# Kernel tuning notes

Hardware: AMD Instinct MI355X
Metric: run time of the kernel (lower is better)

## Reference

```python
import jax, jax.numpy as jnp
import numpy as np
from jax import lax

D_MODEL, D_STATE, D_CONV, EXPAND = 1024, 16, 4, 2
D_INNER = EXPAND * D_MODEL
B, L = 2, 2048


def setup_inputs() -> dict:
    key = jax.random.key(0)
    ks = jax.random.split(key, 8)
    s_in = 1.0 / np.sqrt(D_MODEL)
    s_xp = 1.0 / np.sqrt(D_INNER)
    x = jax.random.normal(ks[0], (B, L, D_MODEL), dtype=jnp.float32)
    W_in = jax.random.uniform(ks[1], (2 * D_INNER, D_MODEL), minval=-s_in, maxval=s_in)
    conv_w = jax.random.uniform(ks[2], (D_INNER, 1, D_CONV), minval=-0.5, maxval=0.5)
    conv_b = jax.random.uniform(ks[3], (D_INNER,), minval=-0.5, maxval=0.5)
    W_xproj = jax.random.uniform(ks[4], (1 + 2 * D_STATE, D_INNER), minval=-s_xp, maxval=s_xp)
    W_dt = jax.random.uniform(ks[5], (D_INNER, 1), minval=-1.0, maxval=1.0)
    b_dt = jax.random.uniform(ks[6], (D_INNER,), minval=-1.0, maxval=1.0)
    A_log = jnp.log(jnp.broadcast_to(jnp.arange(1, D_STATE + 1, dtype=jnp.float32), (D_INNER, D_STATE)))
    D = jnp.ones((D_INNER,), dtype=jnp.float32)
    W_out = jax.random.uniform(ks[7], (D_MODEL, D_INNER), minval=-s_xp, maxval=s_xp)
    return {"x": x, "W_in": W_in, "conv_w": conv_w, "conv_b": conv_b,
            "W_xproj": W_xproj, "W_dt": W_dt, "b_dt": b_dt,
            "A_log": A_log, "D": D, "W_out": W_out}


def reference(x, W_in, conv_w, conv_b, W_xproj, W_dt, b_dt, A_log, D, W_out):
    b, l, _ = x.shape
    d_state = A_log.shape[1]
    d_conv = conv_w.shape[-1]

    xz = x @ W_in.T                                  # (B, L, 2*d_inner)
    x_in, z = jnp.split(xz, 2, axis=-1)

    # causal depthwise conv: torch pads both sides then truncates to [:L]
    lhs = jnp.pad(x_in.transpose(0, 2, 1), ((0, 0), (0, 0), (d_conv - 1, 0)))  # (B, d_inner, L+pad)
    conv = lax.conv_general_dilated(
        lhs, conv_w, window_strides=(1,), padding='VALID',
        dimension_numbers=('NCW', 'OIW', 'NCW'),
        feature_group_count=conv_w.shape[0])
    x_conv = jax.nn.silu(conv.transpose(0, 2, 1) + conv_b)  # (B, L, d_inner)

    ssm_in = x_conv @ W_xproj.T                      # (B, L, 1+2*d_state)
    dt_raw = ssm_in[..., :1]
    B_ssm = ssm_in[..., 1:1 + d_state]               # (B, L, d_state)
    C_ssm = ssm_in[..., 1 + d_state:]                # (B, L, d_state)

    delta = jax.nn.softplus(dt_raw @ W_dt.T + b_dt)  # (B, L, d_inner)
    A = -jnp.exp(A_log)                              # (d_inner, d_state)
    deltaA = jnp.exp(delta[..., None] * A)           # (B, L, d_inner, d_state)
    deltaB_u = delta[..., None] * B_ssm[:, :, None, :] * x_conv[..., None]

    def step(h, inp):
        dA, dBu, c = inp                              # (B,d_inner,d_state)x2, (B,d_state)
        h = dA * h + dBu
        y = jnp.einsum('bds,bs->bd', h, c)
        return h, y

    h0 = jnp.zeros((b, deltaA.shape[2], d_state), dtype=x.dtype)
    _, ys = lax.scan(step, h0, (deltaA.transpose(1, 0, 2, 3),
                                deltaB_u.transpose(1, 0, 2, 3),
                                C_ssm.transpose(1, 0, 2)))
    y = ys.transpose(1, 0, 2) + x_conv * D           # (B, L, d_inner)
    y = y * jax.nn.silu(z)
    return y @ W_out.T
```

## Files before the change

kernel.cpp:

```cpp
#include <hip/hip_runtime.h>
#include <hip/hip_bf16.h>
#include <math.h>

#define D_MODEL 1024
#define D_STATE 16
#define D_CONV  4
#define D_INNER 2048
#define BB      2
#define LL      2048
#define BLROWS  (BB*LL)
#define NCHUNK  64
#define CHUNK   (LL/NCHUNK)
#define SSML    36
#define XSPLIT  16

typedef __hip_bfloat16 bf16;
typedef __attribute__((ext_vector_type(8))) short short8;
typedef __attribute__((ext_vector_type(4))) float f32x4;

__device__ __forceinline__ float ldf(const void* p, long i, int isbf) {
    return isbf ? __bfloat162float(((const bf16*)p)[i]) : ((const float*)p)[i];
}
__device__ __forceinline__ short bfbits(float f) {
    bf16 h = __float2bfloat16(f);
    return *(short*)&h;
}
__device__ __forceinline__ float bits2f(short s) {
    bf16 h; *(short*)&h = s; return __bfloat162float(h);
}
__device__ __forceinline__ float bf2f(bf16 h) { return __bfloat162float(h); }
__device__ __forceinline__ float siluf(float x) {
    return __fdividef(x, 1.f + __expf(-x));
}
__device__ __forceinline__ void softplus_r(float x, float& delta, float& r) {
    float e = __expf(-fabsf(x));
    float t = 1.f + e;
    delta = fmaxf(x, 0.f) + __logf(t);
    r = __fdividef((x >= 0.f) ? e : 1.f, t);
}

#define OFF_CW   0
#define OFF_CB   8192
#define OFF_WDT  10240
#define OFF_BDT  12288
#define OFF_AA   14336
#define OFF_D    47104
#define N_SMALL  49152
#define N_WXPB   (128*2048)
#define N_SSMZ   (BLROWS*SSML)

#define G_LDS16(gptr, lptr) __builtin_amdgcn_global_load_lds( \
    (const __attribute__((address_space(1))) void*)(gptr),    \
    (__attribute__((address_space(3))) void*)(lptr), 16, 0, 0)

__global__ void dtype_probe(const unsigned short* __restrict__ alog, int* __restrict__ flag) {
    if (threadIdx.x == 0) { flag[0] = (alog[1] != 0) ? 1 : 0; flag[1] = 1; }
}

__global__ __launch_bounds__(256) void cvt_prep(
    const void* __restrict__ Wxp, const void* __restrict__ cw,
    const void* __restrict__ cb, const void* __restrict__ wdt,
    const void* __restrict__ bdt, const void* __restrict__ alog,
    const void* __restrict__ Dp,
    bf16* __restrict__ wxpb, float* __restrict__ smallf,
    float* __restrict__ ssm, int* __restrict__ flag)
{
    const int isbf = flag[0];
    int idx = blockIdx.x * 256 + threadIdx.x;
    if (idx < N_WXPB) {
        int row = idx >> 11, col = idx & 2047;
        float v = (row < 33) ? ldf(Wxp, (long)row*2048 + col, isbf) : 0.f;
        wxpb[idx] = __float2bfloat16(v);
        return;
    }
    int j = idx - N_WXPB;
    if      (j < 8192)  smallf[OFF_CW  + j]         = ldf(cw,  j, isbf);
    else if (j < 10240) smallf[OFF_CB  + j - 8192]  = ldf(cb,  j - 8192, isbf);
    else if (j < 12288) smallf[OFF_WDT + j - 10240] = ldf(wdt, j - 10240, isbf);
    else if (j < 14336) smallf[OFF_BDT + j - 12288] = ldf(bdt, j - 12288, isbf);
    else if (j < 47104) {
        int jj = j - 14336;
        float aa = -__expf(ldf(alog, jj, isbf));
        smallf[OFF_AA + jj] = aa;
        int s = jj & 15;
        if (fabsf(aa + (float)(s+1)) > 1e-3f) flag[1] = 0;
    }
    else if (j < 49152) smallf[OFF_D   + j - 47104] = ldf(Dp,  j - 47104, isbf);
    else {
        int z = j - N_SMALL;
        if (z < N_SSMZ) ssm[z] = 0.f;
    }
}

__global__ __launch_bounds__(256) void cvt_all(
    const void* __restrict__ x, const void* __restrict__ win,
    const void* __restrict__ wout,
    bf16* __restrict__ xb, bf16* __restrict__ winb, bf16* __restrict__ woutb,
    const int* __restrict__ flagp)
{
    const int isbf = *flagp;
    int i = blockIdx.x * 256 + threadIdx.x;
    const void* src; bf16* dst; long o;
    if (i < 524288)       { src = x;    dst = xb;    o = (long)i * 8; }
    else if (i < 1048576) { src = win;  dst = winb;  o = (long)(i - 524288) * 8; }
    else if (i < 1310720) { src = wout; dst = woutb; o = (long)(i - 1048576) * 8; }
    else return;
    short8 v;
    if (isbf) {
        v = *(const short8*)((const bf16*)src + o);
    } else {
        const float* s = (const float*)src + o;
        f32x4 u = *(const f32x4*)s, w = *(const f32x4*)(s + 4);
        v[0]=bfbits(u[0]); v[1]=bfbits(u[1]); v[2]=bfbits(u[2]); v[3]=bfbits(u[3]);
        v[4]=bfbits(w[0]); v[5]=bfbits(w[1]); v[6]=bfbits(w[2]); v[7]=bfbits(w[3]);
    }
    *(short8*)(dst + o) = v;
}

__global__ __launch_bounds__(512) void gemm8p(
    const bf16* __restrict__ A,
    const bf16* __restrict__ Bm,
    bf16* __restrict__ Cp)
{
    __shared__ bf16 As[2][256*64];
    __shared__ bf16 Bs[2][256*64];
    const int t    = threadIdx.x;
    const int lane = t & 63;
    const int wm   = (t >> 6) >> 2;
    const int wn   = (t >> 6) & 3;
    const int bm   = blockIdx.y, bn = blockIdx.x;
    const int quad = lane >> 4, l16 = lane & 15;
    const int NST  = 16;

    f32x4 acc[8][4];
    #pragma unroll
    for (int i = 0; i < 8; i++)
        #pragma unroll
        for (int j = 0; j < 4; j++)
            acc[i][j] = f32x4{0.f, 0.f, 0.f, 0.f};

    auto stage = [&](int bufi, int kt) {
        #pragma unroll
        for (int seg = 0; seg < 4; seg++) {
            int s = seg*512 + t, row = s >> 3, sg = s & 7;
            int col = (sg ^ (row & 7)) * 8;
            G_LDS16(A + ((long)bm*256 + row)*1024 + kt*64 + col, &As[bufi][s*8]);
        }
        #pragma unroll
        for (int seg = 0; seg < 4; seg++) {
            int s = seg*512 + t, row = s >> 3, sg = s & 7;
            int col = (sg ^ (row & 7)) * 8;
            G_LDS16(Bm + ((long)bn*256 + row)*1024 + kt*64 + col, &Bs[bufi][s*8]);
        }
    };

    stage(0, 0);
    stage(1, 1);
    asm volatile("s_waitcnt vmcnt(8)" ::: "memory");
    __builtin_amdgcn_s_barrier();

    int cur = 0;
    for (int t0 = 0; t0 < NST; ++t0) {
        short8 af[2][8], bfv[2][4];
        #pragma unroll
        for (int kk = 0; kk < 2; kk++) {
            #pragma unroll
            for (int rt = 0; rt < 8; rt++) {
                int row = wm*128 + rt*16 + l16;
                int c = kk*4 + quad;
                af[kk][rt] = *(const short8*)&As[cur][row*64 + ((c ^ (row & 7))*8)];
            }
            #pragma unroll
            for (int ct = 0; ct < 4; ct++) {
                int row = wn*64 + ct*16 + l16;
                int c = kk*4 + quad;
                bfv[kk][ct] = *(const short8*)&Bs[cur][row*64 + ((c ^ (row & 7))*8)];
            }
        }
        asm volatile("s_waitcnt lgkmcnt(0)" ::: "memory");
        __builtin_amdgcn_sched_barrier(0);
        __builtin_amdgcn_s_barrier();
        __builtin_amdgcn_sched_barrier(0);
        if (t0 + 2 < NST) stage(cur, t0 + 2);
        __builtin_amdgcn_s_setprio(1);
        #pragma unroll
        for (int kk = 0; kk < 2; kk++)
            #pragma unroll
            for (int rt = 0; rt < 8; rt++)
                #pragma unroll
                for (int ct = 0; ct < 4; ct++)
                    acc[rt][ct] = __builtin_amdgcn_mfma_f32_16x16x32_bf16(
                        af[kk][rt], bfv[kk][ct], acc[rt][ct], 0, 0, 0);
        __builtin_amdgcn_s_setprio(0);
        __builtin_amdgcn_sched_barrier(0);
        if (t0 + 2 < NST) { asm volatile("s_waitcnt vmcnt(8)" ::: "memory"); }
        else              { asm volatile("s_waitcnt vmcnt(0)" ::: "memory"); }
        __builtin_amdgcn_sched_barrier(0);
        __builtin_amdgcn_s_barrier();
        cur ^= 1;
    }

    #pragma unroll
    for (int rt = 0; rt < 8; rt++)
        #pragma unroll
        for (int ct = 0; ct < 4; ct++)
            #pragma unroll
            for (int r = 0; r < 4; r++) {
                int row = bm*256 + wm*128 + rt*16 + quad*4 + r;
                int col = bn*256 + wn*64 + ct*16 + l16;
                Cp[(long)row * 4096 + col] = __float2bfloat16(acc[rt][ct][r]);
            }
}

__global__ __launch_bounds__(256) void gemm_dual(
    const void* __restrict__ A, int lda,
    const void* __restrict__ Bm, int ldb,
    void* __restrict__ Cp, int ldc, int K,
    const int* __restrict__ flagp, int amode, int bmode, int cmode)
{
    const int isbf = *flagp;
    const int a_bf = amode ? isbf : 1;
    const int b_bf = bmode ? isbf : 1;
    const int c_bf = cmode ? isbf : 1;

    __shared__ bf16 As[128*64];
    __shared__ bf16 Bs[128*64];
    const int t    = threadIdx.x;
    const int lane = t & 63;
    const int w    = t >> 6;
    const int wm   = w >> 1, wn = w & 1;
    const int bm   = blockIdx.y, bn = blockIdx.x;
    const int quad = lane >> 4, l16 = lane & 15;

    f32x4 acc[4][4];
    #pragma unroll
    for (int i = 0; i < 4; i++)
        #pragma unroll
        for (int j = 0; j < 4; j++)
            acc[i][j] = f32x4{0.f, 0.f, 0.f, 0.f};

    for (int k0 = 0; k0 < K; k0 += 64) {
        __syncthreads();
        if (a_bf) {
            #pragma unroll
            for (int seg = 0; seg < 4; seg++) {
                int s = seg*256 + t, row = s >> 3, sg = s & 7;
                int col = (sg ^ (row & 7)) * 8;
                const bf16* ga = (const bf16*)A + ((long)bm*128 + row)*(long)lda + k0 + col;
                G_LDS16(ga, &As[row*64 + sg*8]);
            }
        } else {
            #pragma unroll
            for (int seg = 0; seg < 4; seg++) {
                int s = seg*256 + t, row = s >> 3, sg = s & 7;
                int col = (sg ^ (row & 7)) * 8;
                const float* ap = (const float*)A + ((long)bm*128 + row)*(long)lda + k0 + col;
                f32x4 u = *(const f32x4*)ap, v = *(const f32x4*)(ap + 4);
                short8 va;
                va[0]=bfbits(u[0]); va[1]=bfbits(u[1]); va[2]=bfbits(u[2]); va[3]=bfbits(u[3]);
                va[4]=bfbits(v[0]); va[5]=bfbits(v[1]); va[6]=bfbits(v[2]); va[7]=bfbits(v[3]);
                *(short8*)&As[row*64 + sg*8] = va;
            }
        }
        if (b_bf) {
            #pragma unroll
            for (int seg = 0; seg < 4; seg++) {
                int s = seg*256 + t, row = s >> 3, sg = s & 7;
                int col = (sg ^ (row & 7)) * 8;
                const bf16* gb = (const bf16*)Bm + ((long)bn*128 + row)*(long)ldb + k0 + col;
                G_LDS16(gb, &Bs[row*64 + sg*8]);
            }
        } else {
            #pragma unroll
            for (int seg = 0; seg < 4; seg++) {
                int s = seg*256 + t, row = s >> 3, sg = s & 7;
                int col = (sg ^ (row & 7)) * 8;
                const float* bp = (const float*)Bm + ((long)bn*128 + row)*(long)ldb + k0 + col;
                f32x4 u = *(const f32x4*)bp, v = *(const f32x4*)(bp + 4);
                short8 vb;
                vb[0]=bfbits(u[0]); vb[1]=bfbits(u[1]); vb[2]=bfbits(u[2]); vb[3]=bfbits(u[3]);
                vb[4]=bfbits(v[0]); vb[5]=bfbits(v[1]); vb[6]=bfbits(v[2]); vb[7]=bfbits(v[3]);
                *(short8*)&Bs[row*64 + sg*8] = vb;
            }
        }
        __syncthreads();

        #pragma unroll
        for (int kk = 0; kk < 64; kk += 32) {
            const int cbase = kk >> 3;
            short8 af[4], bfr[4];
            #pragma unroll
            for (int mi = 0; mi < 4; mi++) {
                int row = wm*64 + mi*16 + l16;
                int c = cbase + quad;
                af[mi] = *(const short8*)&As[row*64 + ((c ^ (row & 7))*8)];
            }
            #pragma unroll
            for (int ni = 0; ni < 4; ni++) {
                int row = wn*64 + ni*16 + l16;
                int c = cbase + quad;
                bfr[ni] = *(const short8*)&Bs[row*64 + ((c ^ (row & 7))*8)];
            }
            #pragma unroll
            for (int mi = 0; mi < 4; mi++)
                #pragma unroll
                for (int ni = 0; ni < 4; ni++)
                    acc[mi][ni] = __builtin_amdgcn_mfma_f32_16x16x32_bf16(
                        af[mi], bfr[ni], acc[mi][ni], 0, 0, 0);
        }
    }

    #pragma unroll
    for (int mi = 0; mi < 4; mi++)
        #pragma unroll
        for (int ni = 0; ni < 4; ni++)
            #pragma unroll
            for (int r = 0; r < 4; r++) {
                int row = bm*128 + wm*64 + mi*16 + quad*4 + r;
                int col = bn*128 + wn*64 + ni*16 + l16;
                float val = acc[mi][ni][r];
                if (c_bf) ((bf16*)Cp)[(long)row * ldc + col] = __float2bfloat16(val);
                else      ((float*)Cp)[(long)row * ldc + col] = val;
            }
}

__global__ __launch_bounds__(256) void gemm_n64(
    const bf16* __restrict__ A, int lda,
    const void* __restrict__ Bm, int ldb,
    void* __restrict__ Cp, int ldc, int K,
    const int* __restrict__ flagp, int bmode, int cmode)
{
    const int isbf = *flagp;
    const int b_bf = bmode ? isbf : 1;
    const int c_bf = cmode ? isbf : 1;

    __shared__ bf16 As[128*64];
    __shared__ bf16 Bs[64*64];
    const int t    = threadIdx.x;
    const int lane = t & 63;
    const int w    = t >> 6;
    const int wm   = w >> 1, wn = w & 1;
    const int bm   = blockIdx.y, bn = blockIdx.x;
    const int quad = lane >> 4, l16 = lane & 15;

    f32x4 acc[4][2];
    #pragma unroll
    for (int i = 0; i < 4; i++)
        #pragma unroll
        for (int j = 0; j < 2; j++)
            acc[i][j] = f32x4{0.f, 0.f, 0.f, 0.f};

    for (int k0 = 0; k0 < K; k0 += 64) {
        __syncthreads();
        #pragma unroll
        for (int seg = 0; seg < 4; seg++) {
            int s = seg*256 + t, row = s >> 3, sg = s & 7;
            int col = (sg ^ (row & 7)) * 8;
            const bf16* ga = A + ((long)bm*128 + row)*(long)lda + k0 + col;
            G_LDS16(ga, &As[row*64 + sg*8]);
        }
        if (b_bf) {
            #pragma unroll
            for (int seg = 0; seg < 2; seg++) {
                int s = seg*256 + t, row = s >> 3, sg = s & 7;
                int col = (sg ^ (row & 7)) * 8;
                const bf16* gb = (const bf16*)Bm + ((long)bn*64 + row)*(long)ldb + k0 + col;
                G_LDS16(gb, &Bs[row*64 + sg*8]);
            }
        } else {
            #pragma unroll
            for (int seg = 0; seg < 2; seg++) {
                int s = seg*256 + t, row = s >> 3, sg = s & 7;
                int col = (sg ^ (row & 7)) * 8;
                const float* bp = (const float*)Bm + ((long)bn*64 + row)*(long)ldb + k0 + col;
                f32x4 u = *(const f32x4*)bp, v = *(const f32x4*)(bp + 4);
                short8 vb;
                vb[0]=bfbits(u[0]); vb[1]=bfbits(u[1]); vb[2]=bfbits(u[2]); vb[3]=bfbits(u[3]);
                vb[4]=bfbits(v[0]); vb[5]=bfbits(v[1]); vb[6]=bfbits(v[2]); vb[7]=bfbits(v[3]);
                *(short8*)&Bs[row*64 + sg*8] = vb;
            }
        }
        __syncthreads();

        #pragma unroll
        for (int kk = 0; kk < 64; kk += 32) {
            const int cbase = kk >> 3;
            short8 af[4], bfr[2];
            #pragma unroll
            for (int mi = 0; mi < 4; mi++) {
                int row = wm*64 + mi*16 + l16;
                int c = cbase + quad;
                af[mi] = *(const short8*)&As[row*64 + ((c ^ (row & 7))*8)];
            }
            #pragma unroll
            for (int ni = 0; ni < 2; ni++) {
                int row = wn*32 + ni*16 + l16;
                int c = cbase + quad;
                bfr[ni] = *(const short8*)&Bs[row*64 + ((c ^ (row & 7))*8)];
            }
            #pragma unroll
            for (int mi = 0; mi < 4; mi++)
                #pragma unroll
                for (int ni = 0; ni < 2; ni++)
                    acc[mi][ni] = __builtin_amdgcn_mfma_f32_16x16x32_bf16(
                        af[mi], bfr[ni], acc[mi][ni], 0, 0, 0);
        }
    }

    #pragma unroll
    for (int mi = 0; mi < 4; mi++)
        #pragma unroll
        for (int ni = 0; ni < 2; ni++)
            #pragma unroll
            for (int r = 0; r < 4; r++) {
                int row = bm*128 + wm*64 + mi*16 + quad*4 + r;
                int col = bn*64 + wn*32 + ni*16 + l16;
                float val = acc[mi][ni][r];
                if (c_bf) ((bf16*)Cp)[(long)row * ldc + col] = __float2bfloat16(val);
                else      ((float*)Cp)[(long)row * ldc + col] = val;
            }
}

__global__ __launch_bounds__(256) void xproj_fused(
    const bf16* __restrict__ xz, const bf16* __restrict__ wxpb,
    const float* __restrict__ smallf, float* __restrict__ ssm)
{
    const float* cwf = smallf + OFF_CW;
    const float* cbf = smallf + OFF_CB;
    __shared__ bf16 As[128*32];
    __shared__ bf16 Bs[128*32];
    const int t    = threadIdx.x;
    const int lane = t & 63;
    const int w    = t >> 6;
    const int wm   = w >> 1, wn = w & 1;
    const int bm   = blockIdx.y;
    const int ks   = blockIdx.x * (D_INNER / XSPLIT);
    const int quad = lane >> 4, l16 = lane & 15;

    f32x4 acc[4][4];
    #pragma unroll
    for (int i = 0; i < 4; i++)
        #pragma unroll
        for (int j = 0; j < 4; j++)
            acc[i][j] = f32x4{0.f, 0.f, 0.f, 0.f};

    for (int k0 = ks; k0 < ks + D_INNER/XSPLIT; k0 += 32) {
        __syncthreads();
        #pragma unroll
        for (int seg = 0; seg < 2; seg++) {
            int s = seg*256 + t, row = s >> 2, dcol = (s & 3) * 8;
            int blg = bm*128 + row;
            int b = blg >> 11, l = blg & (LL - 1);
            int d0 = k0 + dcol;
            float a[8];
            {
                f32x4 c0 = *(const f32x4*)&cbf[d0], c1 = *(const f32x4*)&cbf[d0+4];
                a[0]=c0[0]; a[1]=c0[1]; a[2]=c0[2]; a[3]=c0[3];
                a[4]=c1[0]; a[5]=c1[1]; a[6]=c1[2]; a[7]=c1[3];
            }
            f32x4 cw4[8];
            #pragma unroll
            for (int j = 0; j < 8; j++) cw4[j] = *(const f32x4*)&cwf[(d0+j)*4];
            #pragma unroll
            for (int kk = 0; kk < D_CONV; kk++) {
                int ls = l - 3 + kk;
                if (ls >= 0) {
                    short8 xv = *(const short8*)&xz[((long)(b*LL + ls))*4096 + d0];
                    #pragma unroll
                    for (int j = 0; j < 8; j++) a[j] += bits2f(xv[j]) * cw4[j][kk];
                }
            }
            short8 va;
            #pragma unroll
            for (int j = 0; j < 8; j++) va[j] = bfbits(siluf(a[j]));
            *(short8*)&As[row*32 + dcol] = va;
        }
        #pragma unroll
        for (int seg = 0; seg < 2; seg++) {
            int s = seg*256 + t, row = s >> 2, col = (s & 3) * 8;
            const bf16* gb = wxpb + (long)row*D_INNER + k0 + col;
            G_LDS16(gb, &Bs[row*32 + col]);
        }
        __syncthreads();

        short8 af[4], bfr[4];
        #pragma unroll
        for (int mi = 0; mi < 4; mi++)
            af[mi] = *(const short8*)&As[(wm*64 + mi*16 + l16)*32 + quad*8];
        #pragma unroll
        for (int ni = 0; ni < 4; ni++)
            bfr[ni] = *(const short8*)&Bs[(wn*64 + ni*16 + l16)*32 + quad*8];
        #pragma unroll
        for (int mi = 0; mi < 4; mi++)
            #pragma unroll
            for (int ni = 0; ni < 4; ni++)
                acc[mi][ni] = __builtin_amdgcn_mfma_f32_16x16x32_bf16(
                    af[mi], bfr[ni], acc[mi][ni], 0, 0, 0);
    }

    #pragma unroll
    for (int mi = 0; mi < 4; mi++)
        #pragma unroll
        for (int ni = 0; ni < 4; ni++) {
            int col = wn*64 + ni*16 + l16;
            if (col < 33) {
                int newcol = (col == 0) ? 32 : (col - 1);
                #pragma unroll
                for (int r = 0; r < 4; r++) {
                    int row = bm*128 + wm*64 + mi*16 + quad*4 + r;
                    atomicAdd(&ssm[(long)row * SSML + newcol], acc[mi][ni][r]);
                }
            }
        }
}

template<int CHUNK_T>
__global__ __launch_bounds__(256) void scan_partA(
    const float* __restrict__ ssm, const bf16* __restrict__ xz,
    const float* __restrict__ smallf,
    float* __restrict__ sumdq, float* __restrict__ Q,
    const int* __restrict__ flag)
{
    __shared__ float sL[CHUNK_T*SSML];
    __shared__ bf16  sX[CHUNK_T*256];
    const int fastA = flag[1];
    int d = blockIdx.x * 256 + threadIdx.x;
    int c = blockIdx.y, b = blockIdx.z;
    const int NC = gridDim.y;
    int l0 = c * CHUNK_T;
    {
        const float* src = ssm + (long)(b*LL + l0) * SSML;
        for (int idx = threadIdx.x; idx < CHUNK_T*SSML; idx += 256) sL[idx] = src[idx];
        const bf16* xsrc = xz + (long)(b*LL + l0)*4096 + blockIdx.x*256;
        for (int j = threadIdx.x; j < CHUNK_T*32; j += 256) {
            int li = j >> 5, ln = j & 31;
            *(short8*)&sX[li*256 + ln*8] = *(const short8*)&xsrc[(long)li*4096 + ln*8];
        }
    }
    f32x4 h4[4];
    #pragma unroll
    for (int g = 0; g < 4; g++) h4[g] = f32x4{0.f, 0.f, 0.f, 0.f};
    float Aa[D_STATE];
    if (!fastA) {
        #pragma unroll
        for (int s = 0; s < D_STATE; s++) Aa[s] = smallf[OFF_AA + d*D_STATE + s];
    }
    f32x4 cw4 = *(const f32x4*)&smallf[OFF_CW + d*4];
    float cbv  = smallf[OFF_CB + d];
    float wdt  = smallf[OFF_WDT + d];
    float bdtv = smallf[OFF_BDT + d];
    float win[3];
    #pragma unroll
    for (int k = 0; k < 3; k++) {
        int ls = l0 - 3 + k;
        win[k] = (ls >= 0) ? bf2f(xz[((long)(b*LL + ls))*4096 + d]) : 0.f;
    }
    __syncthreads();
    float sumd = 0.f;
    #pragma unroll 4
    for (int li = 0; li < CHUNK_T; li++) {
        float xnew = bf2f(sX[li*256 + threadIdx.x]);
        float convv = cbv + win[0]*cw4[0] + win[1]*cw4[1] + win[2]*cw4[2] + xnew*cw4[3];
        win[0] = win[1]; win[1] = win[2]; win[2] = xnew;
        float xc = siluf(convv);
        const float* row = &sL[li*SSML];
        f32x4 Bv[4];
        #pragma unroll
        for (int g = 0; g < 4; g++) Bv[g] = *(const f32x4*)(row + g*4);
        float delta, r;
        softplus_r(row[32]*wdt + bdtv, delta, r);
        sumd += delta;
        float du = delta * xc;
        if (fastA) {
            float r2 = r*r;
            float r3 = r2*r;
            float r4 = r2*r2;
            f32x4 p0; p0[0]=r; p0[1]=r2; p0[2]=r3; p0[3]=r4;
            float s8  = r4*r4;
            float s12 = s8*r4;
            h4[0] = p0*h4[0]       + du*Bv[0];
            h4[1] = (p0*r4)*h4[1]  + du*Bv[1];
            h4[2] = (p0*s8)*h4[2]  + du*Bv[2];
            h4[3] = (p0*s12)*h4[3] + du*Bv[3];
        } else {
            #pragma unroll
            for (int g = 0; g < 4; g++)
                #pragma unroll
                for (int j = 0; j < 4; j++) {
                    int s = g*4 + j;
                    h4[g][j] = __expf(delta*Aa[s])*h4[g][j] + du*Bv[g][j];
                }
        }
    }
    sumdq[(long)(b*NC + c)*D_INNER + d] = sumd;
    long o = ((long)(b*NC + c)*D_STATE)*D_INNER + d;
    #pragma unroll
    for (int s = 0; s < D_STATE; s++)
        Q[o + (long)s*D_INNER] = h4[s >> 2][s & 3];
}

__global__ __launch_bounds__(256) void scan_combine(
    const float* __restrict__ sumdq, float* __restrict__ Q_hst,
    const float* __restrict__ smallf, int NC)
{
    int t = blockIdx.x * 256 + threadIdx.x;
    int d = t & (D_INNER - 1);
    int s = (t >> 11) & (D_STATE - 1);
    int b = t >> 15;
    float Aa = smallf[OFF_AA + d*D_STATE + s];
    float h = 0.f;
    #pragma unroll 4
    for (int c = 0; c < NC; c++) {
        float sd = sumdq[(long)(b*NC + c)*D_INNER + d];
        long idx = ((long)(b*NC + c)*D_STATE + s)*D_INNER + d;
        float q = Q_hst[idx];
        Q_hst[idx] = h;
        h = __expf(Aa*sd)*h + q;
    }
}

template<int CHUNK_T>
__global__ __launch_bounds__(256) void scan_partC(
    const float* __restrict__ ssm, bf16* __restrict__ xz,
    const float* __restrict__ smallf, const float* __restrict__ hst,
    const int* __restrict__ flag)
{
    __shared__ float sL[CHUNK_T*SSML];
    __shared__ bf16  sX[CHUNK_T*256];
    __shared__ bf16  sZ[CHUNK_T*256];
    const int fastA = flag[1];
    int d = blockIdx.x * 256 + threadIdx.x;
    int c = blockIdx.y, b = blockIdx.z;
    const int NC = gridDim.y;
    int l0 = c * CHUNK_T;
    {
        const float* src = ssm + (long)(b*LL + l0) * SSML;
        for (int idx = threadIdx.x; idx < CHUNK_T*SSML; idx += 256) sL[idx] = src[idx];
        const bf16* xsrc = xz + (long)(b*LL + l0)*4096 + blockIdx.x*256;
        for (int j = threadIdx.x; j < CHUNK_T*32; j += 256) {
            int li = j >> 5, ln = j & 31;
            *(short8*)&sX[li*256 + ln*8] = *(const short8*)&xsrc[(long)li*4096 + ln*8];
            *(short8*)&sZ[li*256 + ln*8] = *(const short8*)&xsrc[(long)li*4096 + D_INNER + ln*8];
        }
    }
    f32x4 h4[4];
    long o = ((long)(b*NC + c)*D_STATE)*D_INNER + d;
    #pragma unroll
    for (int s = 0; s < D_STATE; s++) h4[s >> 2][s & 3] = hst[o + (long)s*D_INNER];
    float Aa[D_STATE];
    if (!fastA) {
        #pragma unroll
        for (int s = 0; s < D_STATE; s++) Aa[s] = smallf[OFF_AA + d*D_STATE + s];
    }
    f32x4 cw4 = *(const f32x4*)&smallf[OFF_CW + d*4];
    float cbv  = smallf[OFF_CB + d];
    float wdt  = smallf[OFF_WDT + d];
    float bdtv = smallf[OFF_BDT + d];
    float Dv   = smallf[OFF_D + d];
    float win[3];
    #pragma unroll
    for (int k = 0; k < 3; k++) {
        int ls = l0 - 3 + k;
        win[k] = (ls >= 0) ? bf2f(xz[((long)(b*LL + ls))*4096 + d]) : 0.f;
    }
    __syncthreads();
    #pragma unroll 2
    for (int li = 0; li < CHUNK_T; li++) {
        long bl = (long)(b*LL + l0 + li);
        float xnew = bf2f(sX[li*256 + threadIdx.x]);
        float convv = cbv + win[0]*cw4[0] + win[1]*cw4[1] + win[2]*cw4[2] + xnew*cw4[3];
        win[0] = win[1]; win[1] = win[2]; win[2] = xnew;
        float xc = siluf(convv);
        const float* row = &sL[li*SSML];
        f32x4 Bv[4], Cv[4];
        #pragma unroll
        for (int g = 0; g < 4; g++) {
            Bv[g] = *(const f32x4*)(row + g*4);
            Cv[g] = *(const f32x4*)(row + 16 + g*4);
        }
        float delta, r;
        softplus_r(row[32]*wdt + bdtv, delta, r);
        float du = delta * xc;
        f32x4 yacc = f32x4{0.f, 0.f, 0.f, 0.f};
        if (fastA) {
            float r2 = r*r;
            float r3 = r2*r;
            float r4 = r2*r2;
            f32x4 p0; p0[0]=r; p0[1]=r2; p0[2]=r3; p0[3]=r4;
            float s8  = r4*r4;
            float s12 = s8*r4;
            h4[0] = p0*h4[0]       + du*Bv[0];
            h4[1] = (p0*r4)*h4[1]  + du*Bv[1];
            h4[2] = (p0*s8)*h4[2]  + du*Bv[2];
            h4[3] = (p0*s12)*h4[3] + du*Bv[3];
            yacc = yacc + h4[0]*Cv[0];
            yacc = yacc + h4[1]*Cv[1];
            yacc = yacc + h4[2]*Cv[2];
            yacc = yacc + h4[3]*Cv[3];
        } else {
            #pragma unroll
            for (int g = 0; g < 4; g++)
                #pragma unroll
                for (int j = 0; j < 4; j++) {
                    int s = g*4 + j;
                    h4[g][j] = __expf(delta*Aa[s])*h4[g][j] + du*Bv[g][j];
                    yacc[j] += h4[g][j]*Cv[g][j];
                }
        }
        float yv = (yacc[0] + yacc[1]) + (yacc[2] + yacc[3]);
        yv += xc * Dv;
        float z = bf2f(sZ[li*256 + threadIdx.x]);
        yv *= siluf(z);
        xz[bl*4096 + D_INNER + d] = __float2bfloat16(yv);
    }
}

extern "C" void kernel_launch(void* const* d_in, const int* in_sizes, int n_in,
                              void* d_out, int out_size, void* d_ws, size_t ws_size,
                              hipStream_t stream)
{
    char* ws = (char*)d_ws;
    bf16*  xz     = (bf16*) (ws);
    bf16*  wxpb   = (bf16*) (ws + 33554432);
    float* ssm    = (float*)(ws + 34078720);
    float* sumdq  = (float*)(ws + 34668544);
    float* Q      = (float*)(ws + 35717120);
    float* smallf = (float*)(ws + 52494336);
    int*   flag   = (int*)  (ws + 52690944);
    bf16*  woutb  = (bf16*) (ws + 52691008);
    bf16*  xb     = (bf16*) (ws + 35717120);
    bf16*  winb   = (bf16*) (ws + 35717120 + 8388608);
    const bool big = ws_size >= 56885312;

    dtype_probe<<<1, 64, 0, stream>>>((const unsigned short*)d_in[7], flag);

    cvt_prep<<<(N_WXPB + N_SMALL + N_SSMZ)/256, 256, 0, stream>>>(
        d_in[4], d_in[2], d_in[3], d_in[5], d_in[6], d_in[7], d_in[8],
        wxpb, smallf, ssm, flag);

    if (big) {
        cvt_all<<<1310720/256, 256, 0, stream>>>(
            d_in[0], d_in[1], d_in[9], xb, winb, woutb, flag);
        gemm8p<<<dim3(16, 16), 512, 0, stream>>>(xb, winb, xz);
    } else {
        gemm_dual<<<dim3(32, 32), 256, 0, stream>>>(
            d_in[0], D_MODEL, d_in[1], D_MODEL, xz, 2*D_INNER, D_MODEL, flag, 1, 1, 0);
    }

    xproj_fused<<<dim3(XSPLIT, 32), 256, 0, stream>>>(xz, wxpb, smallf, ssm);

    {
        dim3 g(D_INNER/256, NCHUNK, BB);
        scan_partA<CHUNK><<<g, 256, 0, stream>>>(ssm, xz, smallf, sumdq, Q, flag);
        scan_combine<<<(BB*D_STATE*D_INNER)/256, 256, 0, stream>>>(sumdq, Q, smallf, NCHUNK);
        scan_partC<CHUNK><<<g, 256, 0, stream>>>(ssm, xz, smallf, Q, flag);
    }

    if (big) {
        gemm_n64<<<dim3(D_MODEL/64, 32), 256, 0, stream>>>(
            xz + D_INNER, 2*D_INNER, woutb, D_INNER, d_out, D_MODEL, D_INNER, flag, 0, 1);
    } else {
        gemm_n64<<<dim3(D_MODEL/64, 32), 256, 0, stream>>>(
            xz + D_INNER, 2*D_INNER, d_in[9], D_INNER, d_out, D_MODEL, D_INNER, flag, 1, 1);
    }
}
```

Measured before the change: 289.2 us.

## Fuse chunked scan phases into one cooperative kernel with grid syncs

```diff
diff --git a/kernel.cpp b/kernel.cpp
--- a/kernel.cpp
+++ b/kernel.cpp
@@ -1,6 +1,9 @@
 #include <hip/hip_runtime.h>
 #include <hip/hip_bf16.h>
+#include <hip/hip_cooperative_groups.h>
 #include <math.h>
+
+namespace cg = cooperative_groups;
 
 #define D_MODEL 1024
 #define D_STATE 16
@@ -514,6 +517,167 @@
         }
 }
 
+__global__ __launch_bounds__(256) void scan_fused(
+    const float* __restrict__ ssm, bf16* __restrict__ xz,
+    const float* __restrict__ smallf,
+    float* __restrict__ sumdq, float* __restrict__ Q,
+    const int* __restrict__ flag)
+{
+    __shared__ float sL[CHUNK*SSML];
+    __shared__ bf16  sX[CHUNK*256];
+    __shared__ bf16  sZ[CHUNK*256];
+    const int fastA = flag[1];
+    const int d = blockIdx.x * 256 + threadIdx.x;
+    const int c = blockIdx.y, b = blockIdx.z;
+    const int NC = gridDim.y;
+    const int l0 = c * CHUNK;
+    {
+        const float* src = ssm + (long)(b*LL + l0) * SSML;
+        for (int idx = threadIdx.x; idx < CHUNK*SSML; idx += 256) sL[idx] = src[idx];
+        const bf16* xsrc = xz + (long)(b*LL + l0)*4096 + blockIdx.x*256;
+        for (int j = threadIdx.x; j < CHUNK*32; j += 256) {
+            int li = j >> 5, ln = j & 31;
+            *(short8*)&sX[li*256 + ln*8] = *(const short8*)&xsrc[(long)li*4096 + ln*8];
+            *(short8*)&sZ[li*256 + ln*8] = *(const short8*)&xsrc[(long)li*4096 + D_INNER + ln*8];
+        }
+    }
+    f32x4 cw4 = *(const f32x4*)&smallf[OFF_CW + d*4];
+    float cbv  = smallf[OFF_CB + d];
+    float wdt  = smallf[OFF_WDT + d];
+    float bdtv = smallf[OFF_BDT + d];
+    float win0[3];
+    #pragma unroll
+    for (int k = 0; k < 3; k++) {
+        int ls = l0 - 3 + k;
+        win0[k] = (ls >= 0) ? bf2f(xz[((long)(b*LL + ls))*4096 + d]) : 0.f;
+    }
+    __syncthreads();
+
+    {
+        f32x4 h4[4];
+        #pragma unroll
+        for (int g = 0; g < 4; g++) h4[g] = f32x4{0.f, 0.f, 0.f, 0.f};
+        float win[3] = {win0[0], win0[1], win0[2]};
+        float sumd = 0.f;
+        #pragma unroll 4
+        for (int li = 0; li < CHUNK; li++) {
+            float xnew = bf2f(sX[li*256 + threadIdx.x]);
+            float convv = cbv + win[0]*cw4[0] + win[1]*cw4[1] + win[2]*cw4[2] + xnew*cw4[3];
+            win[0] = win[1]; win[1] = win[2]; win[2] = xnew;
+            float xc = siluf(convv);
+            const float* row = &sL[li*SSML];
+            f32x4 Bv[4];
+            #pragma unroll
+            for (int g = 0; g < 4; g++) Bv[g] = *(const f32x4*)(row + g*4);
+            float delta, r;
+            softplus_r(row[32]*wdt + bdtv, delta, r);
+            sumd += delta;
+            float du = delta * xc;
+            if (fastA) {
+                float r2 = r*r, r3 = r2*r, r4 = r2*r2;
+                f32x4 p0; p0[0]=r; p0[1]=r2; p0[2]=r3; p0[3]=r4;
+                float s8 = r4*r4, s12 = s8*r4;
+                h4[0] = p0*h4[0]       + du*Bv[0];
+                h4[1] = (p0*r4)*h4[1]  + du*Bv[1];
+                h4[2] = (p0*s8)*h4[2]  + du*Bv[2];
+                h4[3] = (p0*s12)*h4[3] + du*Bv[3];
+            } else {
+                #pragma unroll
+                for (int g = 0; g < 4; g++)
+                    #pragma unroll
+                    for (int j = 0; j < 4; j++) {
+                        int s = g*4 + j;
+                        h4[g][j] = __expf(delta*smallf[OFF_AA + d*D_STATE + s])*h4[g][j] + du*Bv[g][j];
+                    }
+            }
+        }
+        sumdq[(long)(b*NC + c)*D_INNER + d] = sumd;
+        long o = ((long)(b*NC + c)*D_STATE)*D_INNER + d;
+        #pragma unroll
+        for (int s = 0; s < D_STATE; s++)
+            Q[o + (long)s*D_INNER] = h4[s >> 2][s & 3];
+    }
+
+    cg::this_grid().sync();
+
+    {
+        long lb = ((long)blockIdx.z*gridDim.y + blockIdx.y)*gridDim.x + blockIdx.x;
+        long gt = lb*256 + threadIdx.x;
+        if (gt < (long)BB*D_STATE*D_INNER) {
+            int dd = (int)(gt & (D_INNER - 1));
+            int ss = (int)((gt >> 11) & (D_STATE - 1));
+            int bb = (int)(gt >> 15);
+            float AaC = smallf[OFF_AA + dd*D_STATE + ss];
+            float h = 0.f;
+            #pragma unroll 4
+            for (int c2 = 0; c2 < NCHUNK; c2++) {
+                float sd = sumdq[(long)(bb*NC + c2)*D_INNER + dd];
+                long idx = ((long)(bb*NC + c2)*D_STATE + ss)*D_INNER + dd;
+                float q = Q[idx];
+                Q[idx] = h;
+                h = __expf(AaC*sd)*h + q;
+            }
+        }
+    }
+
+    cg::this_grid().sync();
+
+    {
+        f32x4 h4[4];
+        long o = ((long)(b*NC + c)*D_STATE)*D_INNER + d;
+        #pragma unroll
+        for (int s = 0; s < D_STATE; s++) h4[s >> 2][s & 3] = Q[o + (long)s*D_INNER];
+        float Dv = smallf[OFF_D + d];
+        float win[3] = {win0[0], win0[1], win0[2]};
+        #pragma unroll 2
+        for (int li = 0; li < CHUNK; li++) {
+            long bl = (long)(b*LL + l0 + li);
+            float xnew = bf2f(sX[li*256 + threadIdx.x]);
+            float convv = cbv + win[0]*cw4[0] + win[1]*cw4[1] + win[2]*cw4[2] + xnew*cw4[3];
+            win[0] = win[1]; win[1] = win[2]; win[2] = xnew;
+            float xc = siluf(convv);
+            const float* row = &sL[li*SSML];
+            f32x4 Bv[4], Cv[4];
+            #pragma unroll
+            for (int g = 0; g < 4; g++) {
+                Bv[g] = *(const f32x4*)(row + g*4);
+                Cv[g] = *(const f32x4*)(row + 16 + g*4);
+            }
+            float delta, r;
+            softplus_r(row[32]*wdt + bdtv, delta, r);
+            float du = delta * xc;
+            f32x4 yacc = f32x4{0.f, 0.f, 0.f, 0.f};
+            if (fastA) {
+                float r2 = r*r, r3 = r2*r, r4 = r2*r2;
+                f32x4 p0; p0[0]=r; p0[1]=r2; p0[2]=r3; p0[3]=r4;
+                float s8 = r4*r4, s12 = s8*r4;
+                h4[0] = p0*h4[0]       + du*Bv[0];
+                h4[1] = (p0*r4)*h4[1]  + du*Bv[1];
+                h4[2] = (p0*s8)*h4[2]  + du*Bv[2];
+                h4[3] = (p0*s12)*h4[3] + du*Bv[3];
+                yacc = yacc + h4[0]*Cv[0];
+                yacc = yacc + h4[1]*Cv[1];
+                yacc = yacc + h4[2]*Cv[2];
+                yacc = yacc + h4[3]*Cv[3];
+            } else {
+                #pragma unroll
+                for (int g = 0; g < 4; g++)
+                    #pragma unroll
+                    for (int j = 0; j < 4; j++) {
+                        int s = g*4 + j;
+                        h4[g][j] = __expf(delta*smallf[OFF_AA + d*D_STATE + s])*h4[g][j] + du*Bv[g][j];
+                        yacc[j] += h4[g][j]*Cv[g][j];
+                    }
+            }
+            float yv = (yacc[0] + yacc[1]) + (yacc[2] + yacc[3]);
+            yv += xc * Dv;
+            float z = bf2f(sZ[li*256 + threadIdx.x]);
+            yv *= siluf(z);
+            xz[bl*4096 + D_INNER + d] = __float2bfloat16(yv);
+        }
+    }
+}
+
 template<int CHUNK_T>
 __global__ __launch_bounds__(256) void scan_partA(
     const float* __restrict__ ssm, const bf16* __restrict__ xz,
@@ -572,12 +736,9 @@
         sumd += delta;
         float du = delta * xc;
         if (fastA) {
-            float r2 = r*r;
-            float r3 = r2*r;
-            float r4 = r2*r2;
+            float r2 = r*r, r3 = r2*r, r4 = r2*r2;
             f32x4 p0; p0[0]=r; p0[1]=r2; p0[2]=r3; p0[3]=r4;
-            float s8  = r4*r4;
-            float s12 = s8*r4;
+            float s8 = r4*r4, s12 = s8*r4;
             h4[0] = p0*h4[0]       + du*Bv[0];
             h4[1] = (p0*r4)*h4[1]  + du*Bv[1];
             h4[2] = (p0*s8)*h4[2]  + du*Bv[2];
@@ -683,12 +844,9 @@
         float du = delta * xc;
         f32x4 yacc = f32x4{0.f, 0.f, 0.f, 0.f};
         if (fastA) {
-            float r2 = r*r;
-            float r3 = r2*r;
-            float r4 = r2*r2;
+            float r2 = r*r, r3 = r2*r, r4 = r2*r2;
             f32x4 p0; p0[0]=r; p0[1]=r2; p0[2]=r3; p0[3]=r4;
-            float s8  = r4*r4;
-            float s12 = s8*r4;
+            float s8 = r4*r4, s12 = s8*r4;
             h4[0] = p0*h4[0]       + du*Bv[0];
             h4[1] = (p0*r4)*h4[1]  + du*Bv[1];
             h4[2] = (p0*s8)*h4[2]  + du*Bv[2];
@@ -751,9 +909,17 @@
 
     {
         dim3 g(D_INNER/256, NCHUNK, BB);
-        scan_partA<CHUNK><<<g, 256, 0, stream>>>(ssm, xz, smallf, sumdq, Q, flag);
-        scan_combine<<<(BB*D_STATE*D_INNER)/256, 256, 0, stream>>>(sumdq, Q, smallf, NCHUNK);
-        scan_partC<CHUNK><<<g, 256, 0, stream>>>(ssm, xz, smallf, Q, flag);
+        const float* ssm_c = ssm; const float* smallf_c = smallf;
+        const int* flag_c = flag;
+        void* args[] = { (void*)&ssm_c, (void*)&xz, (void*)&smallf_c,
+                         (void*)&sumdq, (void*)&Q, (void*)&flag_c };
+        hipError_t e = hipLaunchCooperativeKernel(
+            reinterpret_cast<void*>(scan_fused), g, dim3(256, 1, 1), args, 0, stream);
+        if (e != hipSuccess) {
+            scan_partA<CHUNK><<<g, 256, 0, stream>>>(ssm, xz, smallf, sumdq, Q, flag);
+            scan_combine<<<(BB*D_STATE*D_INNER)/256, 256, 0, stream>>>(sumdq, Q, smallf, NCHUNK);
+            scan_partC<CHUNK><<<g, 256, 0, stream>>>(ssm, xz, smallf, Q, flag);
+        }
     }
 
     if (big) {
```

New measurement: 519.1 us. +79.5%, slower.
